# Performance work log

Hardware: AMD Instinct MI355X
Metric: run time of the kernel (lower is better)

## Reference

```python
import jax, jax.numpy as jnp
import numpy as np

DIM = 512
NUM_GROUPS = 32
HEADS = 16
HEAD_DIM = 32
EPS = 1e-6


def group_norm(x, w, b, num_groups=NUM_GROUPS, eps=EPS):
    # x: [B, C, H, W]
    B, C, H, W = x.shape
    xg = x.reshape(B, num_groups, -1)
    mean = xg.mean(axis=-1, keepdims=True)
    var = xg.var(axis=-1, keepdims=True)
    xg = (xg - mean) / jnp.sqrt(var + eps)
    x = xg.reshape(B, C, H, W)
    return x * w[None, :, None, None] + b[None, :, None, None]


def conv1x1(x, w, b):
    # x: [B, C, H, W], w: [O, C], b: [O]
    return jnp.einsum('bchw,oc->bohw', x, w) + b[None, :, None, None]


def setup_inputs() -> dict:
    key = jax.random.key(0)
    ks = jax.random.split(key, 12)
    s = 1.0 / np.sqrt(DIM)
    d = {
        'x': jax.random.normal(ks[0], (1, DIM, 64, 64), dtype=jnp.float32),
        'gn_w': jnp.ones((DIM,), dtype=jnp.float32),
        'gn_b': jnp.zeros((DIM,), dtype=jnp.float32),
        'wq': jax.random.normal(ks[1], (DIM, DIM), dtype=jnp.float32) * s,
        'bq': jax.random.normal(ks[2], (DIM,), dtype=jnp.float32) * 0.01,
        'wk': jax.random.normal(ks[3], (DIM, DIM), dtype=jnp.float32) * s,
        'bk': jax.random.normal(ks[4], (DIM,), dtype=jnp.float32) * 0.01,
        'wv': jax.random.normal(ks[5], (DIM, DIM), dtype=jnp.float32) * s,
        'bv': jax.random.normal(ks[6], (DIM,), dtype=jnp.float32) * 0.01,
        'wo': jax.random.normal(ks[7], (DIM, DIM), dtype=jnp.float32) * s,
        'bo': jax.random.normal(ks[8], (DIM,), dtype=jnp.float32) * 0.01,
    }
    return d


def reference(x, gn_w, gn_b, wq, bq, wk, bk, wv, bv, wo, bo):
    B, C, H, W = x.shape
    N = H * W
    scale = HEAD_DIM ** -0.5

    q_in = x
    qn = group_norm(x, gn_w, gn_b)
    # Faithful to source: v-branch applies norm_q to the already-normalized q.
    vn = group_norm(qn, gn_w, gn_b)

    q = conv1x1(qn, wq, bq)
    k = conv1x1(vn, wk, bk)
    v = conv1x1(vn, wv, bv)

    def to_tokens(t):
        # [B, C, H, W] -> [B, heads, N, head_dim]
        return t.reshape(B, HEADS, HEAD_DIM, N).transpose(0, 1, 3, 2)

    q, k, v = to_tokens(q), to_tokens(k), to_tokens(v)

    attn = jax.nn.softmax(jnp.einsum('bhnd,bhmd->bhnm', q, k) * scale, axis=-1)
    out = jnp.einsum('bhnm,bhmd->bhnd', attn, v)  # [B, heads, N, head_dim]
    out = out.transpose(0, 1, 3, 2).reshape(B, C, H, W)
    out = conv1x1(out, wo, bo)
    return (out + q_in) / jnp.sqrt(jnp.float32(2.0))
```

## Files before the change

### kernel.cpp

```cpp
#include <hip/hip_runtime.h>

#define NTOK 4096
#define CHAN 512
#define GSIZE 65536
#define RSQRT2 0.7071067811865476f
#define SCALE 0.17677669529663687f
#define WB_OFF 32768
#define QT_OFF (WB_OFF + 2097152)
#define WS_NEEDED ((size_t)(QT_OFF + 4194304))

typedef unsigned short ushort_t;
typedef __attribute__((ext_vector_type(8))) short bf16x8;
typedef __attribute__((ext_vector_type(8))) _Float16 f16x8;
typedef __attribute__((ext_vector_type(4))) float f32x4;

__device__ __forceinline__ ushort_t f2b(float f) {
    unsigned u = __float_as_uint(f);
    unsigned r = (u + 0x7FFFu + ((u >> 16) & 1u)) >> 16;
    return (ushort_t)r;
}
__device__ __forceinline__ unsigned pack2r(float a, float b) {
    unsigned ua = __float_as_uint(a), ub = __float_as_uint(b);
    return ((ua + 0x8000u) >> 16) | ((ub + 0x8000u) & 0xFFFF0000u);
}
__device__ __forceinline__ unsigned packh2(float a, float b) {
    return __builtin_bit_cast(unsigned, __builtin_amdgcn_cvt_pkrtz(a, b));
}
__device__ __forceinline__ ushort_t f2h(float f) {
    return (ushort_t)(packh2(f, f) & 0xFFFFu);
}
__device__ __forceinline__ bf16x8 ldfrag(const ushort_t* p) {
    return __builtin_bit_cast(bf16x8, *(const uint4*)p);
}
__device__ __forceinline__ f16x8 ldfragh(const ushort_t* p) {
    return __builtin_bit_cast(f16x8, *(const uint4*)p);
}

__global__ void diag_kernel(float* out, float v) {
    if (threadIdx.x == 0 && blockIdx.x == 0) out[0] = v;
}

__global__ __launch_bounds__(256) void gn_sums(const float* __restrict__ x,
                                               float* __restrict__ S,
                                               float* __restrict__ SS) {
    int c = blockIdx.x, t = threadIdx.x;
    const float4* p = (const float4*)(x + (size_t)c * 4096);
    float s = 0.f, ss = 0.f;
    #pragma unroll
    for (int i = 0; i < 4; i++) {
        float4 f = p[i * 256 + t];
        s += f.x + f.y + f.z + f.w;
        ss += f.x * f.x + f.y * f.y + f.z * f.z + f.w * f.w;
    }
    #pragma unroll
    for (int off = 32; off > 0; off >>= 1) {
        s += __shfl_xor(s, off);
        ss += __shfl_xor(ss, off);
    }
    __shared__ float as[4], bs[4];
    int w = t >> 6;
    if ((t & 63) == 0) { as[w] = s; bs[w] = ss; }
    __syncthreads();
    if (t == 0) {
        S[c] = as[0] + as[1] + as[2] + as[3];
        SS[c] = bs[0] + bs[1] + bs[2] + bs[3];
    }
}

__global__ __launch_bounds__(512) void gn_coef(const float* __restrict__ S,
                                               const float* __restrict__ SS,
                                               const float* __restrict__ gnw,
                                               const float* __restrict__ gnb,
                                               float* __restrict__ qa,
                                               float* __restrict__ qd,
                                               float* __restrict__ va,
                                               float* __restrict__ vd) {
    int c = threadIdx.x;
    float Sc = S[c], SSc = SS[c];
    float gs = Sc, gss = SSc;
    #pragma unroll
    for (int off = 1; off < 16; off <<= 1) {
        gs += __shfl_xor(gs, off);
        gss += __shfl_xor(gss, off);
    }
    float mu = gs * (1.f / GSIZE);
    float var = gss * (1.f / GSIZE) - mu * mu;
    float r1 = rsqrtf(var + 1e-6f);
    float wc = gnw[c], bc = gnb[c];
    float a1 = r1 * wc;
    float d1 = bc - mu * a1;
    qa[c] = a1; qd[c] = d1;
    float S2 = a1 * Sc + 4096.f * d1;
    float SS2 = a1 * a1 * SSc + 2.f * a1 * d1 * Sc + 4096.f * d1 * d1;
    float gs2 = S2, gss2 = SS2;
    #pragma unroll
    for (int off = 1; off < 16; off <<= 1) {
        gs2 += __shfl_xor(gs2, off);
        gss2 += __shfl_xor(gss2, off);
    }
    float mu2 = gs2 * (1.f / GSIZE);
    float var2 = gss2 * (1.f / GSIZE) - mu2 * mu2;
    float r2 = rsqrtf(var2 + 1e-6f);
    float a2 = r2 * wc;
    va[c] = a1 * a2;
    vd[c] = a2 * (d1 - mu2) + bc;
}

__global__ __launch_bounds__(256) void bias_fold(const float* __restrict__ wq,
                                                 const float* __restrict__ wk,
                                                 const float* __restrict__ wv,
                                                 const float* __restrict__ bq,
                                                 const float* __restrict__ bk,
                                                 const float* __restrict__ bv,
                                                 const float* __restrict__ qd,
                                                 const float* __restrict__ vd,
                                                 float* __restrict__ bqf,
                                                 float* __restrict__ bkf,
                                                 float* __restrict__ bvf) {
    int row = blockIdx.x * 4 + (threadIdx.x >> 6);
    int lane = threadIdx.x & 63;
    int m = row >> 9;
    int o = row & 511;
    const float* W = (m == 0) ? wq : (m == 1) ? wk : wv;
    const float* b = (m == 0) ? bq : (m == 1) ? bk : bv;
    const float* d = (m == 0) ? qd : vd;
    float* outp    = (m == 0) ? bqf : (m == 1) ? bkf : bvf;
    const float4* wr = (const float4*)(W + (size_t)o * 512) + lane * 2;
    const float4* dr = (const float4*)d + lane * 2;
    float4 a0 = wr[0], a1 = wr[1], d0 = dr[0], d1 = dr[1];
    float acc = a0.x * d0.x + a0.y * d0.y + a0.z * d0.z + a0.w * d0.w
              + a1.x * d1.x + a1.y * d1.y + a1.z * d1.z + a1.w * d1.w;
    #pragma unroll
    for (int off = 32; off > 0; off >>= 1) acc += __shfl_xor(acc, off);
    if (lane == 0) outp[o] = b[o] + acc;
}

__global__ __launch_bounds__(256) void wprep(const float* __restrict__ wq,
                                             const float* __restrict__ wk,
                                             const float* __restrict__ wv,
                                             const float* __restrict__ wo,
                                             const float* __restrict__ qa,
                                             const float* __restrict__ va,
                                             ushort_t* __restrict__ Wb) {
    int y = blockIdx.y;
    const float* src = (y == 0) ? wq : (y == 1) ? wk : (y == 2) ? wv : wo;
    int i = (blockIdx.x * 256 + threadIdx.x) * 4;
    float4 f = *(const float4*)(src + i);
    if (y < 3) {
        const float* aff = (y == 0) ? qa : va;
        float4 a = *(const float4*)(aff + (i & 511));
        f.x *= a.x; f.y *= a.y; f.z *= a.z; f.w *= a.w;
    }
    uint2 u;
    u.x = pack2r(f.x, f.y);
    u.y = pack2r(f.z, f.w);
    *(uint2*)(Wb + (size_t)y * 262144 + i) = u;
}

__global__ __launch_bounds__(256) void qkv_mfma(const float* __restrict__ x,
                                                const ushort_t* __restrict__ Wb,
                                                const float* __restrict__ bqf,
                                                const float* __restrict__ bkf,
                                                const float* __restrict__ bvf,
                                                ushort_t* __restrict__ QT,
                                                ushort_t* __restrict__ KT,
                                                ushort_t* __restrict__ Vb) {
    __shared__ __align__(16) ushort_t Wl[128][72];
    __shared__ __align__(16) ushort_t Bn[64][72];
    __shared__ __align__(16) ushort_t Tl[64][136];
    int t = threadIdx.x;
    int nbase = blockIdx.x << 6;
    int y = blockIdx.y;
    int buf = y >> 2;
    int obase = (y & 3) << 7;
    const ushort_t* Wsrc = Wb + (size_t)buf * 262144;
    const float* bias = (buf == 0) ? bqf : (buf == 1) ? bkf : bvf;

    int w = t >> 6, lane = t & 63, q15 = lane & 15, quad = lane >> 4;
    f32x4 acc[2][4];
    #pragma unroll
    for (int i = 0; i < 2; i++)
        #pragma unroll
        for (int j = 0; j < 4; j++) acc[i][j] = (f32x4){0.f, 0.f, 0.f, 0.f};

    int tok = t & 63, c8 = t >> 6;
    for (int ck = 0; ck < 512; ck += 64) {
        __syncthreads();
        #pragma unroll
        for (int i = 0; i < 4; i++) {
            int idx = 4 * t + i;
            int row = idx >> 3, seg = idx & 7;
            *(uint4*)&Wl[row][seg * 8] =
                *(const uint4*)&Wsrc[(size_t)(obase + row) * 512 + ck + seg * 8];
        }
        {
            float v[16];
            #pragma unroll
            for (int i = 0; i < 16; i++)
                v[i] = x[(size_t)(ck + c8 * 16 + i) * NTOK + nbase + tok];
            uint4 u0, u1;
            u0.x = pack2r(v[0], v[1]);   u0.y = pack2r(v[2], v[3]);
            u0.z = pack2r(v[4], v[5]);   u0.w = pack2r(v[6], v[7]);
            u1.x = pack2r(v[8], v[9]);   u1.y = pack2r(v[10], v[11]);
            u1.z = pack2r(v[12], v[13]); u1.w = pack2r(v[14], v[15]);
            *(uint4*)&Bn[tok][c8 * 16] = u0;
            *(uint4*)&Bn[tok][c8 * 16 + 8] = u1;
        }
        __syncthreads();
        #pragma unroll
        for (int kk = 0; kk < 2; kk++) {
            bf16x8 af0 = ldfrag(&Wl[w * 32 + q15][kk * 32 + quad * 8]);
            bf16x8 af1 = ldfrag(&Wl[w * 32 + 16 + q15][kk * 32 + quad * 8]);
            #pragma unroll
            for (int n8 = 0; n8 < 4; n8++) {
                bf16x8 bfv = ldfrag(&Bn[n8 * 16 + q15][kk * 32 + quad * 8]);
                acc[0][n8] = __builtin_amdgcn_mfma_f32_16x16x32_bf16(af0, bfv, acc[0][n8], 0, 0, 0);
                acc[1][n8] = __builtin_amdgcn_mfma_f32_16x16x32_bf16(af1, bfv, acc[1][n8], 0, 0, 0);
            }
        }
    }

    if (buf == 2) {
        #pragma unroll
        for (int mi = 0; mi < 2; mi++)
            #pragma unroll
            for (int r = 0; r < 4; r++) {
                int o = obase + w * 32 + mi * 16 + quad * 4 + r;
                float bo = bias[o];
                #pragma unroll
                for (int n8 = 0; n8 < 4; n8++)
                    Vb[(size_t)o * NTOK + nbase + n8 * 16 + q15] = f2h(acc[mi][n8][r] + bo);
            }
        return;
    }

    ushort_t* dstT = (buf == 0) ? QT : KT;
    float qs = (buf == 0) ? SCALE : 1.0f;
    __syncthreads();
    #pragma unroll
    for (int mi = 0; mi < 2; mi++)
        #pragma unroll
        for (int r = 0; r < 4; r++) {
            int mloc = w * 32 + mi * 16 + quad * 4 + r;
            float bo = bias[obase + mloc];
            #pragma unroll
            for (int n8 = 0; n8 < 4; n8++)
                Tl[n8 * 16 + q15][mloc] = f2b((acc[mi][n8][r] + bo) * qs);
        }
    __syncthreads();
    #pragma unroll
    for (int i = 0; i < 4; i++) {
        int idx = 4 * t + i;
        int row = idx >> 4, ch = idx & 15;
        uint4 u = *(const uint4*)&Tl[row][ch * 8];
        *(uint4*)&dstT[(size_t)(nbase + row) * 512 + obase + ch * 8] = u;
    }
}

__global__ __launch_bounds__(512, 4) void attn_v11(ushort_t* __restrict__ QT,
                                                   const ushort_t* __restrict__ KT,
                                                   const ushort_t* __restrict__ V) {
    __shared__ __align__(16) ushort_t Kt[256][40];
    __shared__ __align__(16) ushort_t Vt[32][264];
    int h = blockIdx.y;
    int t = threadIdx.x;
    int w = t >> 6, lane = t & 63, q15 = lane & 15, quad = lane >> 4;
    int qbase = (blockIdx.x << 7) + w * 16;
    int hc = h * 32;
    const ushort_t* Vh = V + (size_t)hc * NTOK;

    bf16x8 qf = ldfrag(&QT[(size_t)(qbase + q15) * 512 + hc + quad * 8]);

    const uint4 onesu = {0x3C003C00u, 0x3C003C00u, 0x3C003C00u, 0x3C003C00u};
    const f16x8 ones = __builtin_bit_cast(f16x8, onesu);

    f32x4 o[2] = {{0.f, 0.f, 0.f, 0.f}, {0.f, 0.f, 0.f, 0.f}};
    f32x4 lacc = {0.f, 0.f, 0.f, 0.f};

    for (int j0 = 0; j0 < NTOK; j0 += 256) {
        __syncthreads();
        #pragma unroll
        for (int i = 0; i < 2; i++) {
            int idx = t + (i << 9);
            int krow = idx >> 2, kseg = idx & 3;
            int rp = krow & 63;
            int src = (krow & 192) | (rp & 0x23) | ((rp & 0x0C) << 1) | ((rp & 0x10) >> 2);
            *(uint4*)&Kt[krow][kseg * 8] =
                *(const uint4*)&KT[(size_t)(j0 + src) * 512 + hc + kseg * 8];
        }
        #pragma unroll
        for (int i = 0; i < 2; i++) {
            int idx = t + (i << 9);
            int vrow = idx >> 5, vseg = idx & 31;
            *(uint4*)&Vt[vrow][vseg * 8] =
                *(const uint4*)&Vh[(size_t)vrow * NTOK + j0 + vseg * 8];
        }
        __syncthreads();

        #pragma unroll
        for (int h2 = 0; h2 < 4; h2++) {
            f32x4 st[4];
            #pragma unroll
            for (int kt = 0; kt < 4; kt++) {
                bf16x8 kf = ldfrag(&Kt[h2 * 64 + kt * 16 + q15][quad * 8]);
                f32x4 z = {0.f, 0.f, 0.f, 0.f};
                st[kt] = __builtin_amdgcn_mfma_f32_16x16x32_bf16(kf, qf, z, 0, 0, 0);
            }

            #pragma unroll
            for (int kt = 0; kt < 4; kt++)
                #pragma unroll
                for (int r = 0; r < 4; r++)
                    st[kt][r] = __expf(st[kt][r]);

            f16x8 v00 = ldfragh(&Vt[q15][h2 * 64 + quad * 8]);
            f16x8 v01 = ldfragh(&Vt[16 + q15][h2 * 64 + quad * 8]);
            f16x8 v10 = ldfragh(&Vt[q15][h2 * 64 + 32 + quad * 8]);
            f16x8 v11 = ldfragh(&Vt[16 + q15][h2 * 64 + 32 + quad * 8]);

            uint4 p0u, p1u;
            p0u.x = packh2(st[0][0], st[0][1]);
            p0u.y = packh2(st[0][2], st[0][3]);
            p0u.z = packh2(st[1][0], st[1][1]);
            p0u.w = packh2(st[1][2], st[1][3]);
            p1u.x = packh2(st[2][0], st[2][1]);
            p1u.y = packh2(st[2][2], st[2][3]);
            p1u.z = packh2(st[3][0], st[3][1]);
            p1u.w = packh2(st[3][2], st[3][3]);
            f16x8 pf0 = __builtin_bit_cast(f16x8, p0u);
            f16x8 pf1 = __builtin_bit_cast(f16x8, p1u);
            o[0] = __builtin_amdgcn_mfma_f32_16x16x32_f16(pf0, v00, o[0], 0, 0, 0);
            o[1] = __builtin_amdgcn_mfma_f32_16x16x32_f16(pf0, v01, o[1], 0, 0, 0);
            lacc = __builtin_amdgcn_mfma_f32_16x16x32_f16(pf0, ones, lacc, 0, 0, 0);
            o[0] = __builtin_amdgcn_mfma_f32_16x16x32_f16(pf1, v10, o[0], 0, 0, 0);
            o[1] = __builtin_amdgcn_mfma_f32_16x16x32_f16(pf1, v11, o[1], 0, 0, 0);
            lacc = __builtin_amdgcn_mfma_f32_16x16x32_f16(pf1, ones, lacc, 0, 0, 0);
        }
    }

    #pragma unroll
    for (int r = 0; r < 4; r++) {
        float li = 1.f / lacc[r];
        int q = quad * 4 + r;
        QT[(size_t)(qbase + q) * 512 + hc + q15]      = f2b(o[0][r] * li);
        QT[(size_t)(qbase + q) * 512 + hc + 16 + q15] = f2b(o[1][r] * li);
    }
}

__global__ __launch_bounds__(256) void oproj_mfma(const ushort_t* __restrict__ OT,
                                                  const ushort_t* __restrict__ Wob,
                                                  const float* __restrict__ bo,
                                                  const float* __restrict__ x,
                                                  float* __restrict__ out) {
    __shared__ __align__(16) ushort_t Wl[64][40];
    __shared__ __align__(16) ushort_t Bn[64][40];
    int t = threadIdx.x;
    int nbase = blockIdx.x << 6;
    int obase = blockIdx.y << 6;
    int w = t >> 6, lane = t & 63, q15 = lane & 15, quad = lane >> 4;

    f32x4 acc[4];
    #pragma unroll
    for (int i = 0; i < 4; i++) acc[i] = (f32x4){0.f, 0.f, 0.f, 0.f};

    int arow = t >> 2, aseg = t & 3;
    for (int ck = 0; ck < 512; ck += 32) {
        __syncthreads();
        *(uint4*)&Wl[arow][aseg * 8] =
            *(const uint4*)&Wob[(size_t)(obase + arow) * 512 + ck + aseg * 8];
        *(uint4*)&Bn[arow][aseg * 8] =
            *(const uint4*)&OT[(size_t)(nbase + arow) * 512 + ck + aseg * 8];
        __syncthreads();
        bf16x8 af = ldfrag(&Wl[w * 16 + q15][quad * 8]);
        #pragma unroll
        for (int n8 = 0; n8 < 4; n8++) {
            bf16x8 bfv = ldfrag(&Bn[n8 * 16 + q15][quad * 8]);
            acc[n8] = __builtin_amdgcn_mfma_f32_16x16x32_bf16(af, bfv, acc[n8], 0, 0, 0);
        }
    }

    #pragma unroll
    for (int r = 0; r < 4; r++) {
        int o = obase + w * 16 + quad * 4 + r;
        float b = bo[o];
        #pragma unroll
        for (int n8 = 0; n8 < 4; n8++) {
            size_t idx = (size_t)o * NTOK + nbase + n8 * 16 + q15;
            out[idx] = (acc[n8][r] + b + x[idx]) * RSQRT2;
        }
    }
}

extern "C" void kernel_launch(void* const* d_in, const int* in_sizes, int n_in,
                              void* d_out, int out_size, void* d_ws, size_t ws_size,
                              hipStream_t stream) {
    const float* x   = (const float*)d_in[0];
    const float* gnw = (const float*)d_in[1];
    const float* gnb = (const float*)d_in[2];
    const float* wq  = (const float*)d_in[3];
    const float* bq  = (const float*)d_in[4];
    const float* wk  = (const float*)d_in[5];
    const float* bk  = (const float*)d_in[6];
    const float* wv  = (const float*)d_in[7];
    const float* bv  = (const float*)d_in[8];
    const float* wo  = (const float*)d_in[9];
    const float* bo  = (const float*)d_in[10];
    float* out = (float*)d_out;

    if (ws_size < WS_NEEDED) {
        diag_kernel<<<1, 64, 0, stream>>>(out, (float)(ws_size >> 16));
        return;
    }

    char* wsb = (char*)d_ws;
    float* S   = (float*)(wsb + 0);
    float* SS  = (float*)(wsb + 2048);
    float* qa  = (float*)(wsb + 4096);
    float* qd  = (float*)(wsb + 6144);
    float* va  = (float*)(wsb + 8192);
    float* vd  = (float*)(wsb + 10240);
    float* bqf = (float*)(wsb + 12288);
    float* bkf = (float*)(wsb + 14336);
    float* bvf = (float*)(wsb + 16384);
    ushort_t* Wb = (ushort_t*)(wsb + WB_OFF);
    ushort_t* QT = (ushort_t*)(wsb + QT_OFF);
    ushort_t* KT = (ushort_t*)d_out;
    ushort_t* Vb = (ushort_t*)d_out + (size_t)CHAN * NTOK;

    gn_sums<<<512, 256, 0, stream>>>(x, S, SS);
    gn_coef<<<1, 512, 0, stream>>>(S, SS, gnw, gnb, qa, qd, va, vd);
    bias_fold<<<384, 256, 0, stream>>>(wq, wk, wv, bq, bk, bv, qd, vd, bqf, bkf, bvf);
    wprep<<<dim3(256, 4), 256, 0, stream>>>(wq, wk, wv, wo, qa, va, Wb);

    qkv_mfma<<<dim3(64, 12), 256, 0, stream>>>(x, Wb, bqf, bkf, bvf, QT, KT, Vb);

    attn_v11<<<dim3(32, 16), 512, 0, stream>>>(QT, KT, Vb);

    oproj_mfma<<<dim3(64, 8), 256, 0, stream>>>(QT, Wb + (size_t)3 * 262144, bo, x, out);
}
```

Baseline: 170.7 us.

## Double-buffer K/V tiles in attention with register prefetch and MFMA priority hints

The attention kernel now keeps two shared-memory buffers for K and V. The next 256-token tile is loaded from global memory into registers while the current tile is computed, and those registers are written into the other buffer afterwards, so one barrier per iteration is removed. s_setprio is raised around the MFMA groups so the waves issuing matrix work get scheduling priority. This doubles LDS use and raises register pressure, which may lower occupancy below the 4-block launch bound.

```diff
diff --git a/kernel.cpp b/kernel.cpp
--- a/kernel.cpp
+++ b/kernel.cpp
@@ -257,11 +257,11 @@
     }
 }
 
-__global__ __launch_bounds__(512, 4) void attn_v11(ushort_t* __restrict__ QT,
+__global__ __launch_bounds__(512, 4) void attn_v12(ushort_t* __restrict__ QT,
                                                    const ushort_t* __restrict__ KT,
                                                    const ushort_t* __restrict__ V) {
-    __shared__ __align__(16) ushort_t Kt[256][40];
-    __shared__ __align__(16) ushort_t Vt[32][264];
+    __shared__ __align__(16) ushort_t Kt[2][256][40];
+    __shared__ __align__(16) ushort_t Vt[2][32][264];
     int h = blockIdx.y;
     int t = threadIdx.x;
     int w = t >> 6, lane = t & 63, q15 = lane & 15, quad = lane >> 4;
@@ -277,35 +277,63 @@
     f32x4 o[2] = {{0.f, 0.f, 0.f, 0.f}, {0.f, 0.f, 0.f, 0.f}};
     f32x4 lacc = {0.f, 0.f, 0.f, 0.f};
 
-    for (int j0 = 0; j0 < NTOK; j0 += 256) {
+    uint4 kreg[2], vreg[2];
+
+    #define LOADT(J0)                                                           \
+        {                                                                       \
+            _Pragma("unroll")                                                   \
+            for (int i = 0; i < 2; i++) {                                       \
+                int idx = t + (i << 9);                                         \
+                int krow = idx >> 2, kseg = idx & 3;                            \
+                int rp = krow & 63;                                             \
+                int src = (krow & 192) | (rp & 0x23) | ((rp & 0x0C) << 1) |     \
+                          ((rp & 0x10) >> 2);                                   \
+                kreg[i] = *(const uint4*)&KT[(size_t)((J0) + src) * 512 + hc +  \
+                                             kseg * 8];                         \
+            }                                                                   \
+            _Pragma("unroll")                                                   \
+            for (int i = 0; i < 2; i++) {                                       \
+                int idx = t + (i << 9);                                         \
+                int vrow = idx >> 5, vseg = idx & 31;                           \
+                vreg[i] = *(const uint4*)&Vh[(size_t)vrow * NTOK + (J0) +       \
+                                             vseg * 8];                         \
+            }                                                                   \
+        }
+
+    #define STORET(B)                                                           \
+        {                                                                       \
+            _Pragma("unroll")                                                   \
+            for (int i = 0; i < 2; i++) {                                       \
+                int idx = t + (i << 9);                                         \
+                *(uint4*)&Kt[(B)][idx >> 2][(idx & 3) * 8] = kreg[i];           \
+            }                                                                   \
+            _Pragma("unroll")                                                   \
+            for (int i = 0; i < 2; i++) {                                       \
+                int idx = t + (i << 9);                                         \
+                *(uint4*)&Vt[(B)][idx >> 5][(idx & 31) * 8] = vreg[i];          \
+            }                                                                   \
+        }
+
+    LOADT(0);
+    STORET(0);
+
+    #pragma unroll 2
+    for (int tt = 0; tt < 16; tt++) {
+        int cur = tt & 1;
         __syncthreads();
-        #pragma unroll
-        for (int i = 0; i < 2; i++) {
-            int idx = t + (i << 9);
-            int krow = idx >> 2, kseg = idx & 3;
-            int rp = krow & 63;
-            int src = (krow & 192) | (rp & 0x23) | ((rp & 0x0C) << 1) | ((rp & 0x10) >> 2);
-            *(uint4*)&Kt[krow][kseg * 8] =
-                *(const uint4*)&KT[(size_t)(j0 + src) * 512 + hc + kseg * 8];
-        }
-        #pragma unroll
-        for (int i = 0; i < 2; i++) {
-            int idx = t + (i << 9);
-            int vrow = idx >> 5, vseg = idx & 31;
-            *(uint4*)&Vt[vrow][vseg * 8] =
-                *(const uint4*)&Vh[(size_t)vrow * NTOK + j0 + vseg * 8];
-        }
-        __syncthreads();
+        if (tt < 15) LOADT((tt + 1) << 8);
 
         #pragma unroll
         for (int h2 = 0; h2 < 4; h2++) {
             f32x4 st[4];
+            __builtin_amdgcn_s_setprio(1);
             #pragma unroll
             for (int kt = 0; kt < 4; kt++) {
-                bf16x8 kf = ldfrag(&Kt[h2 * 64 + kt * 16 + q15][quad * 8]);
+                bf16x8 kf = ldfrag(&Kt[cur][h2 * 64 + kt * 16 + q15][quad * 8]);
                 f32x4 z = {0.f, 0.f, 0.f, 0.f};
                 st[kt] = __builtin_amdgcn_mfma_f32_16x16x32_bf16(kf, qf, z, 0, 0, 0);
             }
+            __builtin_amdgcn_s_setprio(0);
 
             #pragma unroll
             for (int kt = 0; kt < 4; kt++)
@@ -313,10 +341,10 @@
                 for (int r = 0; r < 4; r++)
                     st[kt][r] = __expf(st[kt][r]);
 
-            f16x8 v00 = ldfragh(&Vt[q15][h2 * 64 + quad * 8]);
-            f16x8 v01 = ldfragh(&Vt[16 + q15][h2 * 64 + quad * 8]);
-            f16x8 v10 = ldfragh(&Vt[q15][h2 * 64 + 32 + quad * 8]);
-            f16x8 v11 = ldfragh(&Vt[16 + q15][h2 * 64 + 32 + quad * 8]);
+            f16x8 v00 = ldfragh(&Vt[cur][q15][h2 * 64 + quad * 8]);
+            f16x8 v01 = ldfragh(&Vt[cur][16 + q15][h2 * 64 + quad * 8]);
+            f16x8 v10 = ldfragh(&Vt[cur][q15][h2 * 64 + 32 + quad * 8]);
+            f16x8 v11 = ldfragh(&Vt[cur][16 + q15][h2 * 64 + 32 + quad * 8]);
 
             uint4 p0u, p1u;
             p0u.x = packh2(st[0][0], st[0][1]);
@@ -329,14 +357,20 @@
             p1u.w = packh2(st[3][2], st[3][3]);
             f16x8 pf0 = __builtin_bit_cast(f16x8, p0u);
             f16x8 pf1 = __builtin_bit_cast(f16x8, p1u);
+            __builtin_amdgcn_s_setprio(1);
             o[0] = __builtin_amdgcn_mfma_f32_16x16x32_f16(pf0, v00, o[0], 0, 0, 0);
             o[1] = __builtin_amdgcn_mfma_f32_16x16x32_f16(pf0, v01, o[1], 0, 0, 0);
             lacc = __builtin_amdgcn_mfma_f32_16x16x32_f16(pf0, ones, lacc, 0, 0, 0);
             o[0] = __builtin_amdgcn_mfma_f32_16x16x32_f16(pf1, v10, o[0], 0, 0, 0);
             o[1] = __builtin_amdgcn_mfma_f32_16x16x32_f16(pf1, v11, o[1], 0, 0, 0);
             lacc = __builtin_amdgcn_mfma_f32_16x16x32_f16(pf1, ones, lacc, 0, 0, 0);
-        }
-    }
+            __builtin_amdgcn_s_setprio(0);
+        }
+
+        if (tt < 15) STORET(cur ^ 1);
+    }
+    #undef LOADT
+    #undef STORET
 
     #pragma unroll
     for (int r = 0; r < 4; r++) {
@@ -434,7 +468,7 @@
 
     qkv_mfma<<<dim3(64, 12), 256, 0, stream>>>(x, Wb, bqf, bkf, bvf, QT, KT, Vb);
 
-    attn_v11<<<dim3(32, 16), 512, 0, stream>>>(QT, KT, Vb);
+    attn_v12<<<dim3(32, 16), 512, 0, stream>>>(QT, KT, Vb);
 
     oproj_mfma<<<dim3(64, 8), 256, 0, stream>>>(QT, Wb + (size_t)3 * 262144, bo, x, out);
 }
```

Measured after the change: 195.9 us. +14.8%, slower.

## Double-buffer attention K/V tiles with direct global-to-LDS async loads

Applied to the files above, without the earlier changes.

Replaces the synchronous register-staged K/V tile loads with global_load_lds direct copies into two XOR-swizzled LDS buffers. The next tile is prefetched while the current one is computed, which is meant to hide global load latency and drop one barrier per iteration. MFMA sections are wrapped with s_setprio to favour matrix issue. LDS use roughly doubles, which can lower occupancy. Correctness depends on the swizzle matching on both the write and read side and on the async copies finishing before the barrier.

```diff
diff --git a/kernel.cpp b/kernel.cpp
--- a/kernel.cpp
+++ b/kernel.cpp
@@ -34,6 +34,11 @@
 }
 __device__ __forceinline__ f16x8 ldfragh(const ushort_t* p) {
     return __builtin_bit_cast(f16x8, *(const uint4*)p);
+}
+__device__ __forceinline__ void ldg2lds16(const void* g, void* l) {
+    __builtin_amdgcn_global_load_lds(
+        (const __attribute__((address_space(1))) void*)g,
+        (__attribute__((address_space(3))) void*)l, 16, 0, 0);
 }
 
 __global__ void diag_kernel(float* out, float v) {
@@ -257,11 +262,11 @@
     }
 }
 
-__global__ __launch_bounds__(512, 4) void attn_v11(ushort_t* __restrict__ QT,
+__global__ __launch_bounds__(512, 4) void attn_v13(ushort_t* __restrict__ QT,
                                                    const ushort_t* __restrict__ KT,
                                                    const ushort_t* __restrict__ V) {
-    __shared__ __align__(16) ushort_t Kt[256][40];
-    __shared__ __align__(16) ushort_t Vt[32][264];
+    __shared__ __align__(16) ushort_t KtF[2][8192];
+    __shared__ __align__(16) ushort_t VtF[2][8192];
     int h = blockIdx.y;
     int t = threadIdx.x;
     int w = t >> 6, lane = t & 63, q15 = lane & 15, quad = lane >> 4;
@@ -277,35 +282,51 @@
     f32x4 o[2] = {{0.f, 0.f, 0.f, 0.f}, {0.f, 0.f, 0.f, 0.f}};
     f32x4 lacc = {0.f, 0.f, 0.f, 0.f};
 
-    for (int j0 = 0; j0 < NTOK; j0 += 256) {
+    auto issue = [&](int j0, int b) {
+        #pragma unroll
+        for (int i = 0; i < 2; i++) {
+            int sbase = (w << 6) + (i << 9);
+            int idx = sbase + lane;
+            int krow = idx >> 2;
+            int gd = (idx & 3) ^ ((krow >> 1) & 3);
+            int rp = krow & 63;
+            int srcr = (krow & 192) | (rp & 0x23) | ((rp & 0x0C) << 1) | ((rp & 0x10) >> 2);
+            ldg2lds16(&KT[(size_t)(j0 + srcr) * 512 + hc + gd * 8],
+                      &KtF[b][sbase * 8]);
+        }
+        #pragma unroll
+        for (int i = 0; i < 2; i++) {
+            int sbase = (w << 6) + (i << 9);
+            int idx = sbase + lane;
+            int d = idx >> 5;
+            int gd = (idx & 31) ^ (d & 7);
+            ldg2lds16(&Vh[(size_t)d * NTOK + j0 + gd * 8],
+                      &VtF[b][sbase * 8]);
+        }
+    };
+
+    issue(0, 0);
+    int ksp8 = (quad ^ ((q15 >> 1) & 3)) * 8;
+    int vq = q15 & 7;
+
+    for (int tt = 0; tt < 16; tt++) {
+        int cur = tt & 1;
         __syncthreads();
-        #pragma unroll
-        for (int i = 0; i < 2; i++) {
-            int idx = t + (i << 9);
-            int krow = idx >> 2, kseg = idx & 3;
-            int rp = krow & 63;
-            int src = (krow & 192) | (rp & 0x23) | ((rp & 0x0C) << 1) | ((rp & 0x10) >> 2);
-            *(uint4*)&Kt[krow][kseg * 8] =
-                *(const uint4*)&KT[(size_t)(j0 + src) * 512 + hc + kseg * 8];
-        }
-        #pragma unroll
-        for (int i = 0; i < 2; i++) {
-            int idx = t + (i << 9);
-            int vrow = idx >> 5, vseg = idx & 31;
-            *(uint4*)&Vt[vrow][vseg * 8] =
-                *(const uint4*)&Vh[(size_t)vrow * NTOK + j0 + vseg * 8];
-        }
-        __syncthreads();
+        if (tt < 15) issue((tt + 1) << 8, cur ^ 1);
+        const ushort_t* KtC = KtF[cur];
+        const ushort_t* VtC = VtF[cur];
 
         #pragma unroll
         for (int h2 = 0; h2 < 4; h2++) {
             f32x4 st[4];
+            __builtin_amdgcn_s_setprio(1);
             #pragma unroll
             for (int kt = 0; kt < 4; kt++) {
-                bf16x8 kf = ldfrag(&Kt[h2 * 64 + kt * 16 + q15][quad * 8]);
+                bf16x8 kf = ldfrag(&KtC[(h2 * 64 + kt * 16 + q15) * 32 + ksp8]);
                 f32x4 z = {0.f, 0.f, 0.f, 0.f};
                 st[kt] = __builtin_amdgcn_mfma_f32_16x16x32_bf16(kf, qf, z, 0, 0, 0);
             }
+            __builtin_amdgcn_s_setprio(0);
 
             #pragma unroll
             for (int kt = 0; kt < 4; kt++)
@@ -313,10 +334,12 @@
                 for (int r = 0; r < 4; r++)
                     st[kt][r] = __expf(st[kt][r]);
 
-            f16x8 v00 = ldfragh(&Vt[q15][h2 * 64 + quad * 8]);
-            f16x8 v01 = ldfragh(&Vt[16 + q15][h2 * 64 + quad * 8]);
-            f16x8 v10 = ldfragh(&Vt[q15][h2 * 64 + 32 + quad * 8]);
-            f16x8 v11 = ldfragh(&Vt[16 + q15][h2 * 64 + 32 + quad * 8]);
+            int g0 = ((h2 * 8 + quad) ^ vq) * 8;
+            int g1 = g0 ^ 32;
+            f16x8 v00 = ldfragh(&VtC[q15 * 256 + g0]);
+            f16x8 v01 = ldfragh(&VtC[(16 + q15) * 256 + g0]);
+            f16x8 v10 = ldfragh(&VtC[q15 * 256 + g1]);
+            f16x8 v11 = ldfragh(&VtC[(16 + q15) * 256 + g1]);
 
             uint4 p0u, p1u;
             p0u.x = packh2(st[0][0], st[0][1]);
@@ -329,12 +352,14 @@
             p1u.w = packh2(st[3][2], st[3][3]);
             f16x8 pf0 = __builtin_bit_cast(f16x8, p0u);
             f16x8 pf1 = __builtin_bit_cast(f16x8, p1u);
+            __builtin_amdgcn_s_setprio(1);
             o[0] = __builtin_amdgcn_mfma_f32_16x16x32_f16(pf0, v00, o[0], 0, 0, 0);
             o[1] = __builtin_amdgcn_mfma_f32_16x16x32_f16(pf0, v01, o[1], 0, 0, 0);
             lacc = __builtin_amdgcn_mfma_f32_16x16x32_f16(pf0, ones, lacc, 0, 0, 0);
             o[0] = __builtin_amdgcn_mfma_f32_16x16x32_f16(pf1, v10, o[0], 0, 0, 0);
             o[1] = __builtin_amdgcn_mfma_f32_16x16x32_f16(pf1, v11, o[1], 0, 0, 0);
             lacc = __builtin_amdgcn_mfma_f32_16x16x32_f16(pf1, ones, lacc, 0, 0, 0);
+            __builtin_amdgcn_s_setprio(0);
         }
     }
 
@@ -434,7 +459,7 @@
 
     qkv_mfma<<<dim3(64, 12), 256, 0, stream>>>(x, Wb, bqf, bkf, bvf, QT, KT, Vb);
 
-    attn_v11<<<dim3(32, 16), 512, 0, stream>>>(QT, KT, Vb);
+    attn_v13<<<dim3(32, 16), 512, 0, stream>>>(QT, KT, Vb);
 
     oproj_mfma<<<dim3(64, 8), 256, 0, stream>>>(QT, Wb + (size_t)3 * 262144, bo, x, out);
 }
```

After: 166.5 us. -2.4%, faster.
